# Performance work log

Measured on AMD Instinct MI355X. Metric: run time of the kernel, lower is better.

The kernel has to match this reference:

```python
import jax, jax.numpy as jnp
import numpy as np

S, N, M = 8, 4096, 64          # snapshots, atoms, total neighbors (sum of max_num_neighs)
L = 20.0                        # periodic box length
R_CS, R_C = 2.0, 6.0            # smooth cutoff radii
DSUB = 16                       # dim_sub_net
PAD_FRAC = 0.15                 # fraction of -1 padded neighbor slots


def _mlp(x, params):
    # DenseChainNet: Linear -> relu between layers, no activation after last layer
    n = len(params)
    for i, (W, b) in enumerate(params):
        x = x @ W + b
        if i < n - 1:
            x = jax.nn.relu(x)
    return x


def _lin(k, fan_in, fan_out):
    k1, k2 = jax.random.split(k)
    s = 1.0 / np.sqrt(fan_in)
    W = jax.random.uniform(k1, (fan_in, fan_out), minval=-s, maxval=s, dtype=jnp.float32)
    b = jax.random.uniform(k2, (fan_out,), minval=-s, maxval=s, dtype=jnp.float32)
    return W, b


def setup_inputs() -> dict:
    key = jax.random.key(0)
    ks = jax.random.split(key, 12)
    inputs = jax.random.uniform(ks[0], (S, N, 3), dtype=jnp.float32) * L
    input_types = jax.random.randint(ks[1], (S, N), 0, 2)
    # neighbor indices, guaranteed != self, with -1 padding
    base = jnp.arange(N, dtype=jnp.int32)[None, :, None]
    off = jax.random.randint(ks[2], (S, N, M), 1, N)
    neigh = (base + off) % N
    pad = jax.random.uniform(ks[3], (S, N, M)) < PAD_FRAC
    neigh_list = jnp.where(pad, -1, neigh).astype(jnp.int32)
    es1_w, es1_b = _lin(ks[4], 2, 4)
    es2_w, es2_b = _lin(ks[5], 4, 4)
    fs1_w, fs1_b = _lin(ks[6], 4, 4)
    fs2_w, fs2_b = _lin(ks[7], 4, 4)
    en1_w, en1_b = _lin(ks[8], 4, 8)
    en2_w, en2_b = _lin(ks[9], 8, 16)
    en3_w, en3_b = _lin(ks[10], 16, 32)
    return dict(inputs=inputs, input_types=input_types, neigh_list=neigh_list,
                es1_w=es1_w, es1_b=es1_b, es2_w=es2_w, es2_b=es2_b,
                fs1_w=fs1_w, fs1_b=fs1_b, fs2_w=fs2_w, fs2_b=fs2_b,
                en1_w=en1_w, en1_b=en1_b, en2_w=en2_w, en2_b=en2_b,
                en3_w=en3_w, en3_b=en3_b)


def reference(inputs, input_types, neigh_list,
              es1_w, es1_b, es2_w, es2_b,
              fs1_w, fs1_b, fs2_w, fs2_b,
              en1_w, en1_b, en2_w, en2_b, en3_w, en3_b):
    mask = neigh_list == -1                               # [S,N,M]
    idx = jnp.where(mask, 0, neigh_list)
    flat = idx.reshape(S, N * M)
    # gather neighbor coordinates with periodic minimum-image convention
    pos_j = jnp.take_along_axis(inputs, flat[..., None], axis=1).reshape(S, N, M, 3)
    d = pos_j - inputs[:, :, None, :]
    d = d - L * jnp.round(d / L)
    r = jnp.sqrt(jnp.sum(d * d, axis=-1) + 1e-12)         # [S,N,M]
    # smooth cutoff: s(r) = 1/r for r<r_cs, cosine switch to 0 at r_c
    u = (r - R_CS) / (R_C - R_CS)
    sw = jnp.where(r < R_CS, 1.0,
                   jnp.where(r < R_C, 0.5 * jnp.cos(jnp.pi * u) + 0.5, 0.0))
    s_ij = jnp.where(mask, 0.0, sw / r)                   # [S,N,M]
    r_ij = d * (s_ij / r)[..., None]                      # s(r) * d / r, [S,N,M,3]
    # species pair descriptor (symmetrized over pair order)
    neigh_types = jnp.take_along_axis(input_types, flat, axis=1).reshape(S, N, M)
    self_t = jnp.broadcast_to(input_types[:, :, None], (S, N, M))
    pairs = jnp.stack([self_t, neigh_types], axis=-1).astype(jnp.float32).reshape(-1, 2)
    es = [(es1_w, es1_b), (es2_w, es2_b)]
    td = _mlp(pairs, es) + _mlp(pairs[:, ::-1], es)
    td = _mlp(td, [(fs1_w, fs1_b), (fs2_w, fs2_b)]).reshape(S, N, M, -1)  # [S,N,M,4]
    s_tilde = (td * s_ij[..., None]).reshape(S * N * M, -1)
    G = _mlp(s_tilde, [(en1_w, en1_b), (en2_w, en2_b), (en3_w, en3_b)]).reshape(S, N, M, -1)  # [S,N,M,32]
    r_tilde = jnp.concatenate([s_ij[..., None], r_ij], axis=-1)            # [S,N,M,4]
    R = jnp.einsum('snmd,snmk->sndk', r_tilde, G[..., :DSUB])              # [S,N,4,16]
    R1 = jnp.einsum('snmd,sndk->snmk', r_tilde, R)                         # [S,N,M,16]
    D = jnp.einsum('snmg,snmk->sngk', G, R1)                               # [S,N,32,16]
    return D
```

## Files before the change

### kernel.cpp

```cpp
#include <hip/hip_runtime.h>
#include <math.h>

#define SS 8
#define NN 4096
#define MM 64
#define LBOX 20.0f

typedef __attribute__((ext_vector_type(8))) short short8;
typedef __attribute__((ext_vector_type(4))) float floatx4;

__device__ inline unsigned short f2bf(float x) {
    unsigned u = __float_as_uint(x);
    u += 0x7fffu + ((u >> 16) & 1u);
    return (unsigned short)(u >> 16);
}

__global__ __launch_bounds__(256) void desc_kernel(
    const float* __restrict__ pos,
    const int*   __restrict__ types,
    const int*   __restrict__ neigh,
    const float* __restrict__ es1_w, const float* __restrict__ es1_b,
    const float* __restrict__ es2_w, const float* __restrict__ es2_b,
    const float* __restrict__ fs1_w, const float* __restrict__ fs1_b,
    const float* __restrict__ fs2_w, const float* __restrict__ fs2_b,
    const float* __restrict__ en1_w, const float* __restrict__ en1_b,
    const float* __restrict__ en2_w, const float* __restrict__ en2_b,
    const float* __restrict__ en3_w, const float* __restrict__ en3_b,
    float* __restrict__ out)
{
    __shared__ alignas(16) unsigned short sh_h2[4][16][72];
    __shared__ alignas(16) unsigned short sh_rt[4][4][72];
    __shared__ alignas(16) float sh_PT[4][4][20];
    __shared__ alignas(16) float sh_W3t[32][20];
    __shared__ alignas(16) float sh_A[4][128];
    __shared__ alignas(16) float sh_vt[4][8];
    __shared__ float sh_b3[32];

    const int tid = threadIdx.x;

    if (tid < 4) {
        const float ti = (float)(tid >> 1), tj = (float)(tid & 1);
        float e[4] = {0.f, 0.f, 0.f, 0.f};
        #pragma unroll
        for (int swp = 0; swp < 2; ++swp) {
            const float a = swp ? tj : ti, b = swp ? ti : tj;
            float h[4];
            #pragma unroll
            for (int k = 0; k < 4; ++k)
                h[k] = fmaxf(a * es1_w[k] + b * es1_w[4 + k] + es1_b[k], 0.f);
            #pragma unroll
            for (int k = 0; k < 4; ++k) {
                float acc = es2_b[k];
                #pragma unroll
                for (int j = 0; j < 4; ++j) acc += h[j] * es2_w[j * 4 + k];
                e[k] += acc;
            }
        }
        float f[4];
        #pragma unroll
        for (int k = 0; k < 4; ++k) {
            float acc = fs1_b[k];
            #pragma unroll
            for (int j = 0; j < 4; ++j) acc += e[j] * fs1_w[j * 4 + k];
            f[k] = fmaxf(acc, 0.f);
        }
        float td[4];
        #pragma unroll
        for (int k = 0; k < 4; ++k) {
            float acc = fs2_b[k];
            #pragma unroll
            for (int j = 0; j < 4; ++j) acc += f[j] * fs2_w[j * 4 + k];
            td[k] = acc;
        }
        #pragma unroll
        for (int o = 0; o < 8; ++o) {
            float acc = 0.f;
            #pragma unroll
            for (int d = 0; d < 4; ++d) acc += td[d] * en1_w[d * 8 + o];
            sh_vt[tid][o] = acc;
        }
    }
    {
        int i = tid;
        sh_W3t[i & 31][i >> 5] = en3_w[i];
        i += 256;
        sh_W3t[i & 31][i >> 5] = en3_w[i];
    }
    if (tid < 32) sh_b3[tid] = en3_b[tid];
    __syncthreads();

    const int wave = tid >> 6;
    const int lane = tid & 63;
    const int atom = blockIdx.x * 4 + wave;
    const int sbase = atom & ~(NN - 1);

    const float xi = pos[atom * 3 + 0];
    const float yi = pos[atom * 3 + 1];
    const float zi = pos[atom * 3 + 2];
    const int   ti = types[atom];

    const int nb  = neigh[atom * MM + lane];
    const int msk = nb < 0;
    const int j   = msk ? 0 : nb;
    const int gj  = sbase + j;

    float dx = pos[gj * 3 + 0] - xi;
    float dy = pos[gj * 3 + 1] - yi;
    float dz = pos[gj * 3 + 2] - zi;
    dx -= LBOX * rintf(dx * (1.0f / LBOX));
    dy -= LBOX * rintf(dy * (1.0f / LBOX));
    dz -= LBOX * rintf(dz * (1.0f / LBOX));
    const float r2   = fmaf(dx, dx, fmaf(dy, dy, fmaf(dz, dz, 1e-12f)));
    const float rinv = rsqrtf(r2);
    const float r    = r2 * rinv;
    const float u    = (r - 2.0f) * 0.25f;
    float swv = 0.5f * __cosf(3.14159265358979323846f * u) + 0.5f;
    swv = (r < 2.0f) ? 1.0f : ((r < 6.0f) ? swv : 0.0f);
    const float sij   = msk ? 0.0f : swv * rinv;
    const float scale = sij * rinv;

    const int tj = types[gj];
    const int tt = ti * 2 + tj;

    float h1[8];
    {
        const float4 va = *(const float4*)(&sh_vt[tt][0]);
        const float4 vb = *(const float4*)(&sh_vt[tt][4]);
        h1[0] = fmaxf(fmaf(sij, va.x, en1_b[0]), 0.f);
        h1[1] = fmaxf(fmaf(sij, va.y, en1_b[1]), 0.f);
        h1[2] = fmaxf(fmaf(sij, va.z, en1_b[2]), 0.f);
        h1[3] = fmaxf(fmaf(sij, va.w, en1_b[3]), 0.f);
        h1[4] = fmaxf(fmaf(sij, vb.x, en1_b[4]), 0.f);
        h1[5] = fmaxf(fmaf(sij, vb.y, en1_b[5]), 0.f);
        h1[6] = fmaxf(fmaf(sij, vb.z, en1_b[6]), 0.f);
        h1[7] = fmaxf(fmaf(sij, vb.w, en1_b[7]), 0.f);
    }

    #pragma unroll
    for (int k = 0; k < 16; ++k) {
        float acc = en2_b[k];
        #pragma unroll
        for (int i = 0; i < 8; ++i) acc = fmaf(h1[i], en2_w[i * 16 + k], acc);
        sh_h2[wave][k][lane] = f2bf(fmaxf(acc, 0.f));
    }
    sh_rt[wave][0][lane] = f2bf(sij);
    sh_rt[wave][1][lane] = f2bf(dx * scale);
    sh_rt[wave][2][lane] = f2bf(dy * scale);
    sh_rt[wave][3][lane] = f2bf(dz * scale);
    __syncthreads();

    const int col = lane & 15;
    const int q4  = lane >> 4;
    const int m0  = q4 * 8;
    floatx4 cP = {0.f, 0.f, 0.f, 0.f};
    floatx4 cQ = {0.f, 0.f, 0.f, 0.f};
    const short8 ones = (short8)(short)0x3F80;
    #pragma unroll
    for (int ck = 0; ck < 2; ++ck) {
        const short8 af = *(const short8*)&sh_h2[wave][col][ck * 32 + m0];
        const short8 bf = *(const short8*)&sh_rt[wave][col & 3][ck * 32 + m0];
        cP = __builtin_amdgcn_mfma_f32_16x16x32_bf16(af, bf, cP, 0, 0, 0);
        cQ = __builtin_amdgcn_mfma_f32_16x16x32_bf16(ones, bf, cQ, 0, 0, 0);
    }
    if (col < 4) *(floatx4*)&sh_PT[wave][col][q4 * 4] = cP;
    const float qd = cQ[0];
    __syncthreads();

    {
        const int g0 = lane >> 2, dd = lane & 3, g1 = g0 + 16;
        float a0 = sh_b3[g0] * qd;
        float a1 = sh_b3[g1] * qd;
        #pragma unroll
        for (int c = 0; c < 4; ++c) {
            const floatx4 pv = *(const floatx4*)&sh_PT[wave][dd][c * 4];
            const floatx4 w0 = *(const floatx4*)&sh_W3t[g0][c * 4];
            const floatx4 w1 = *(const floatx4*)&sh_W3t[g1][c * 4];
            a0 = fmaf(pv.x, w0.x, a0); a0 = fmaf(pv.y, w0.y, a0);
            a0 = fmaf(pv.z, w0.z, a0); a0 = fmaf(pv.w, w0.w, a0);
            a1 = fmaf(pv.x, w1.x, a1); a1 = fmaf(pv.y, w1.y, a1);
            a1 = fmaf(pv.z, w1.z, a1); a1 = fmaf(pv.w, w1.w, a1);
        }
        sh_A[wave][lane]      = a0;
        sh_A[wave][lane + 64] = a1;
    }
    __syncthreads();

    {
        const int g = lane >> 1, koff = (lane & 1) * 8;
        const float4 Ag = *(const float4*)&sh_A[wave][g * 4];
        float o[8];
        #pragma unroll
        for (int jj = 0; jj < 8; ++jj) {
            const float4 Ak = *(const float4*)&sh_A[wave][(koff + jj) * 4];
            o[jj] = fmaf(Ag.x, Ak.x, fmaf(Ag.y, Ak.y, fmaf(Ag.z, Ak.z, Ag.w * Ak.w)));
        }
        float* op = out + (size_t)atom * 512 + lane * 8;
        *(float4*)(op)     = make_float4(o[0], o[1], o[2], o[3]);
        *(float4*)(op + 4) = make_float4(o[4], o[5], o[6], o[7]);
    }
}

extern "C" void kernel_launch(void* const* d_in, const int* in_sizes, int n_in,
                              void* d_out, int out_size, void* d_ws, size_t ws_size,
                              hipStream_t stream) {
    const float* pos   = (const float*)d_in[0];
    const int*   typ   = (const int*)d_in[1];
    const int*   ngh   = (const int*)d_in[2];
    desc_kernel<<<dim3((SS * NN) / 4), dim3(256), 0, stream>>>(
        pos, typ, ngh,
        (const float*)d_in[3],  (const float*)d_in[4],
        (const float*)d_in[5],  (const float*)d_in[6],
        (const float*)d_in[7],  (const float*)d_in[8],
        (const float*)d_in[9],  (const float*)d_in[10],
        (const float*)d_in[11], (const float*)d_in[12],
        (const float*)d_in[13], (const float*)d_in[14],
        (const float*)d_in[15], (const float*)d_in[16],
        (float*)d_out);
}
```

Before: 130.5 us.

## Move en2 layer to MFMA and replace block barriers with wave-local waits

The per-lane scalar 8x16 en2 layer becomes two 32x32x16 bf16 MFMAs, with the bias folded in as an extra weight row, and the results are written packed to LDS. The three block-wide __syncthreads after the setup phase become s_waitcnt lgkmcnt(0), relying on each wave touching only its own LDS slice. The code also uses hardware bf16 conversion, a clamped switch-function argument instead of branches, packed float2 FMAs with a re-laid-out W3, readfirstlane for the wave and atom indices, and nontemporal output stores. Dropping the barriers saves synchronisation but depends on the LDS ordering within a wave holding.

```diff
diff --git a/kernel.cpp b/kernel.cpp
--- a/kernel.cpp
+++ b/kernel.cpp
@@ -6,13 +6,20 @@
 #define MM 64
 #define LBOX 20.0f
 
-typedef __attribute__((ext_vector_type(8))) short short8;
-typedef __attribute__((ext_vector_type(4))) float floatx4;
-
-__device__ inline unsigned short f2bf(float x) {
-    unsigned u = __float_as_uint(x);
-    u += 0x7fffu + ((u >> 16) & 1u);
-    return (unsigned short)(u >> 16);
+typedef __attribute__((ext_vector_type(8)))  short    short8;
+typedef __attribute__((ext_vector_type(2)))  float    floatx2;
+typedef __attribute__((ext_vector_type(4)))  float    floatx4;
+typedef __attribute__((ext_vector_type(16))) float    floatx16;
+typedef __attribute__((ext_vector_type(2)))  unsigned uintx2;
+typedef __attribute__((ext_vector_type(2)))  __bf16   bf16x2;
+
+__device__ inline unsigned pkbf(float a, float b) {
+    bf16x2 p; p.x = (__bf16)a; p.y = (__bf16)b;
+    unsigned u; __builtin_memcpy(&u, &p, 4); return u;
+}
+__device__ inline unsigned short bfbits(float x) {
+    __bf16 b = (__bf16)x;
+    unsigned short u; __builtin_memcpy(&u, &b, 2); return u;
 }
 
 __global__ __launch_bounds__(256) void desc_kernel(
@@ -28,13 +35,14 @@
     const float* __restrict__ en3_w, const float* __restrict__ en3_b,
     float* __restrict__ out)
 {
+    __shared__ alignas(16) unsigned short sh_W2x[2][16][8];
     __shared__ alignas(16) unsigned short sh_h2[4][16][72];
     __shared__ alignas(16) unsigned short sh_rt[4][4][72];
     __shared__ alignas(16) float sh_PT[4][4][20];
-    __shared__ alignas(16) float sh_W3t[32][20];
+    __shared__ alignas(16) float sh_W3p[512];
+    __shared__ alignas(16) float sh_b3p[16][2];
     __shared__ alignas(16) float sh_A[4][128];
     __shared__ alignas(16) float sh_vt[4][8];
-    __shared__ float sh_b3[32];
 
     const int tid = threadIdx.x;
 
@@ -81,17 +89,22 @@
         }
     }
     {
-        int i = tid;
-        sh_W3t[i & 31][i >> 5] = en3_w[i];
-        i += 256;
-        sh_W3t[i & 31][i >> 5] = en3_w[i];
-    }
-    if (tid < 32) sh_b3[tid] = en3_b[tid];
+        const int q = tid >> 7, col = (tid >> 3) & 15, j = tid & 7;
+        const float wv = q ? (j == 0 ? en2_b[col] : 0.f) : en2_w[j * 16 + col];
+        sh_W2x[q][col][j] = bfbits(wv);
+    }
+    #pragma unroll
+    for (int rr = 0; rr < 2; ++rr) {
+        const int i = tid + rr * 256;
+        const int hp = i >> 6, g = (i >> 2) & 15, w = i & 3;
+        sh_W3p[i] = en3_w[(2 * hp + (w >> 1)) * 32 + g + 16 * (w & 1)];
+    }
+    if (tid < 32) sh_b3p[tid >> 1][tid & 1] = en3_b[(tid & 1) * 16 + (tid >> 1)];
     __syncthreads();
 
-    const int wave = tid >> 6;
+    const int wave = __builtin_amdgcn_readfirstlane(tid >> 6);
     const int lane = tid & 63;
-    const int atom = blockIdx.x * 4 + wave;
+    const int atom = __builtin_amdgcn_readfirstlane(blockIdx.x * 4 + (tid >> 6));
     const int sbase = atom & ~(NN - 1);
 
     const float xi = pos[atom * 3 + 0];
@@ -101,102 +114,129 @@
 
     const int nb  = neigh[atom * MM + lane];
     const int msk = nb < 0;
-    const int j   = msk ? 0 : nb;
-    const int gj  = sbase + j;
-
-    float dx = pos[gj * 3 + 0] - xi;
-    float dy = pos[gj * 3 + 1] - yi;
-    float dz = pos[gj * 3 + 2] - zi;
+    const int gj  = sbase + (msk ? 0 : nb);
+
+    const float* pj = pos + gj * 3;
+    float dx = pj[0] - xi;
+    float dy = pj[1] - yi;
+    float dz = pj[2] - zi;
     dx -= LBOX * rintf(dx * (1.0f / LBOX));
     dy -= LBOX * rintf(dy * (1.0f / LBOX));
     dz -= LBOX * rintf(dz * (1.0f / LBOX));
     const float r2   = fmaf(dx, dx, fmaf(dy, dy, fmaf(dz, dz, 1e-12f)));
     const float rinv = rsqrtf(r2);
     const float r    = r2 * rinv;
-    const float u    = (r - 2.0f) * 0.25f;
-    float swv = 0.5f * __cosf(3.14159265358979323846f * u) + 0.5f;
-    swv = (r < 2.0f) ? 1.0f : ((r < 6.0f) ? swv : 0.0f);
+    const float u    = fminf(fmaxf((r - 2.0f) * 0.25f, 0.0f), 1.0f);
+    const float swv  = 0.5f * __cosf(3.14159265358979323846f * u) + 0.5f;
     const float sij   = msk ? 0.0f : swv * rinv;
     const float scale = sij * rinv;
 
     const int tj = types[gj];
     const int tt = ti * 2 + tj;
 
-    float h1[8];
+    unsigned hp[4];
     {
         const float4 va = *(const float4*)(&sh_vt[tt][0]);
         const float4 vb = *(const float4*)(&sh_vt[tt][4]);
-        h1[0] = fmaxf(fmaf(sij, va.x, en1_b[0]), 0.f);
-        h1[1] = fmaxf(fmaf(sij, va.y, en1_b[1]), 0.f);
-        h1[2] = fmaxf(fmaf(sij, va.z, en1_b[2]), 0.f);
-        h1[3] = fmaxf(fmaf(sij, va.w, en1_b[3]), 0.f);
-        h1[4] = fmaxf(fmaf(sij, vb.x, en1_b[4]), 0.f);
-        h1[5] = fmaxf(fmaf(sij, vb.y, en1_b[5]), 0.f);
-        h1[6] = fmaxf(fmaf(sij, vb.z, en1_b[6]), 0.f);
-        h1[7] = fmaxf(fmaf(sij, vb.w, en1_b[7]), 0.f);
-    }
-
+        const float h0 = fmaxf(fmaf(sij, va.x, en1_b[0]), 0.f);
+        const float h1v= fmaxf(fmaf(sij, va.y, en1_b[1]), 0.f);
+        const float h2v= fmaxf(fmaf(sij, va.z, en1_b[2]), 0.f);
+        const float h3 = fmaxf(fmaf(sij, va.w, en1_b[3]), 0.f);
+        const float h4 = fmaxf(fmaf(sij, vb.x, en1_b[4]), 0.f);
+        const float h5 = fmaxf(fmaf(sij, vb.y, en1_b[5]), 0.f);
+        const float h6 = fmaxf(fmaf(sij, vb.z, en1_b[6]), 0.f);
+        const float h7 = fmaxf(fmaf(sij, vb.w, en1_b[7]), 0.f);
+        hp[0] = pkbf(h0, h1v); hp[1] = pkbf(h2v, h3);
+        hp[2] = pkbf(h4, h5);  hp[3] = pkbf(h6, h7);
+    }
+
+    const int q2 = lane >> 5;
+    union U { unsigned u[4]; short8 v; } a0, a1;
     #pragma unroll
-    for (int k = 0; k < 16; ++k) {
-        float acc = en2_b[k];
-        #pragma unroll
-        for (int i = 0; i < 8; ++i) acc = fmaf(h1[i], en2_w[i * 16 + k], acc);
-        sh_h2[wave][k][lane] = f2bf(fmaxf(acc, 0.f));
-    }
-    sh_rt[wave][0][lane] = f2bf(sij);
-    sh_rt[wave][1][lane] = f2bf(dx * scale);
-    sh_rt[wave][2][lane] = f2bf(dy * scale);
-    sh_rt[wave][3][lane] = f2bf(dz * scale);
-    __syncthreads();
-
-    const int col = lane & 15;
-    const int q4  = lane >> 4;
-    const int m0  = q4 * 8;
+    for (int i = 0; i < 4; ++i) {
+        const unsigned other = (unsigned)__shfl_xor((int)hp[i], 32, 64);
+        const unsigned bias  = (i == 0) ? 0x3F80u : 0u;
+        a0.u[i] = q2 ? bias : hp[i];
+        a1.u[i] = q2 ? bias : other;
+    }
+    const short8 bw = *(const short8*)&sh_W2x[q2][lane & 15][0];
+    floatx16 c0 = {}, c1 = {};
+    c0 = __builtin_amdgcn_mfma_f32_32x32x16_bf16(a0.v, bw, c0, 0, 0, 0);
+    c1 = __builtin_amdgcn_mfma_f32_32x32x16_bf16(a1.v, bw, c1, 0, 0, 0);
+
+    const int col32 = lane & 31;
+    if (col32 < 16) {
+        unsigned short* row = &sh_h2[wave][col32][0];
+        #pragma unroll
+        for (int g = 0; g < 4; ++g) {
+            const int m = 8 * g + 4 * q2;
+            uintx2 w0, w1;
+            w0.x = pkbf(fmaxf(c0[4*g+0], 0.f), fmaxf(c0[4*g+1], 0.f));
+            w0.y = pkbf(fmaxf(c0[4*g+2], 0.f), fmaxf(c0[4*g+3], 0.f));
+            *(uintx2*)(row + m) = w0;
+            w1.x = pkbf(fmaxf(c1[4*g+0], 0.f), fmaxf(c1[4*g+1], 0.f));
+            w1.y = pkbf(fmaxf(c1[4*g+2], 0.f), fmaxf(c1[4*g+3], 0.f));
+            *(uintx2*)(row + 32 + m) = w1;
+        }
+    }
+    {
+        const unsigned p0 = pkbf(sij, dx * scale), p1 = pkbf(dy * scale, dz * scale);
+        sh_rt[wave][0][lane] = (unsigned short)p0;
+        sh_rt[wave][1][lane] = (unsigned short)(p0 >> 16);
+        sh_rt[wave][2][lane] = (unsigned short)p1;
+        sh_rt[wave][3][lane] = (unsigned short)(p1 >> 16);
+    }
+    asm volatile("s_waitcnt lgkmcnt(0)" ::: "memory");
+
+    const int col16 = lane & 15;
+    const int q4    = lane >> 4;
+    const int m0    = q4 * 8;
     floatx4 cP = {0.f, 0.f, 0.f, 0.f};
     floatx4 cQ = {0.f, 0.f, 0.f, 0.f};
     const short8 ones = (short8)(short)0x3F80;
     #pragma unroll
     for (int ck = 0; ck < 2; ++ck) {
-        const short8 af = *(const short8*)&sh_h2[wave][col][ck * 32 + m0];
-        const short8 bf = *(const short8*)&sh_rt[wave][col & 3][ck * 32 + m0];
+        const short8 af = *(const short8*)&sh_h2[wave][col16][ck * 32 + m0];
+        const short8 bf = *(const short8*)&sh_rt[wave][col16 & 3][ck * 32 + m0];
         cP = __builtin_amdgcn_mfma_f32_16x16x32_bf16(af, bf, cP, 0, 0, 0);
         cQ = __builtin_amdgcn_mfma_f32_16x16x32_bf16(ones, bf, cQ, 0, 0, 0);
     }
-    if (col < 4) *(floatx4*)&sh_PT[wave][col][q4 * 4] = cP;
+    if (col16 < 4) *(floatx4*)&sh_PT[wave][col16][q4 * 4] = cP;
     const float qd = cQ[0];
-    __syncthreads();
-
-    {
-        const int g0 = lane >> 2, dd = lane & 3, g1 = g0 + 16;
-        float a0 = sh_b3[g0] * qd;
-        float a1 = sh_b3[g1] * qd;
-        #pragma unroll
-        for (int c = 0; c < 4; ++c) {
-            const floatx4 pv = *(const floatx4*)&sh_PT[wave][dd][c * 4];
-            const floatx4 w0 = *(const floatx4*)&sh_W3t[g0][c * 4];
-            const floatx4 w1 = *(const floatx4*)&sh_W3t[g1][c * 4];
-            a0 = fmaf(pv.x, w0.x, a0); a0 = fmaf(pv.y, w0.y, a0);
-            a0 = fmaf(pv.z, w0.z, a0); a0 = fmaf(pv.w, w0.w, a0);
-            a1 = fmaf(pv.x, w1.x, a1); a1 = fmaf(pv.y, w1.y, a1);
-            a1 = fmaf(pv.z, w1.z, a1); a1 = fmaf(pv.w, w1.w, a1);
-        }
-        sh_A[wave][lane]      = a0;
-        sh_A[wave][lane + 64] = a1;
-    }
-    __syncthreads();
+    asm volatile("s_waitcnt lgkmcnt(0)" ::: "memory");
+
+    {
+        const int g0 = lane >> 2, dd = lane & 3;
+        const floatx2 b3v = *(const floatx2*)&sh_b3p[g0][0];
+        floatx2 acc2 = floatx2{qd, qd} * b3v;
+        #pragma unroll
+        for (int h4 = 0; h4 < 4; ++h4) {
+            const floatx4 pv = *(const floatx4*)&sh_PT[wave][dd][h4 * 4];
+            const floatx4 wa = *(const floatx4*)&sh_W3p[(h4 * 2 + 0) * 64 + g0 * 4];
+            const floatx4 wb = *(const floatx4*)&sh_W3p[(h4 * 2 + 1) * 64 + g0 * 4];
+            acc2 += floatx2{pv.x, pv.x} * floatx2{wa.x, wa.y};
+            acc2 += floatx2{pv.y, pv.y} * floatx2{wa.z, wa.w};
+            acc2 += floatx2{pv.z, pv.z} * floatx2{wb.x, wb.y};
+            acc2 += floatx2{pv.w, pv.w} * floatx2{wb.z, wb.w};
+        }
+        sh_A[wave][lane]      = acc2.x;
+        sh_A[wave][lane + 64] = acc2.y;
+    }
+    asm volatile("s_waitcnt lgkmcnt(0)" ::: "memory");
 
     {
         const int g = lane >> 1, koff = (lane & 1) * 8;
-        const float4 Ag = *(const float4*)&sh_A[wave][g * 4];
-        float o[8];
+        const floatx4 Ag = *(const floatx4*)&sh_A[wave][g * 4];
+        floatx4 o0, o1;
         #pragma unroll
         for (int jj = 0; jj < 8; ++jj) {
-            const float4 Ak = *(const float4*)&sh_A[wave][(koff + jj) * 4];
-            o[jj] = fmaf(Ag.x, Ak.x, fmaf(Ag.y, Ak.y, fmaf(Ag.z, Ak.z, Ag.w * Ak.w)));
+            const floatx4 Ak = *(const floatx4*)&sh_A[wave][(koff + jj) * 4];
+            const float v = fmaf(Ag.x, Ak.x, fmaf(Ag.y, Ak.y, fmaf(Ag.z, Ak.z, Ag.w * Ak.w)));
+            if (jj < 4) o0[jj] = v; else o1[jj - 4] = v;
         }
         float* op = out + (size_t)atom * 512 + lane * 8;
-        *(float4*)(op)     = make_float4(o[0], o[1], o[2], o[3]);
-        *(float4*)(op + 4) = make_float4(o[4], o[5], o[6], o[7]);
+        __builtin_nontemporal_store(o0, (floatx4*)op);
+        __builtin_nontemporal_store(o1, (floatx4*)(op + 4));
     }
 }
 
```

Result: no change. 133.0 us (+1.9%).
